# Optimization experiments

Hardware: AMD Instinct MI355X
Metric: run time of the kernel (lower is better)

## Reference

```python
import jax, jax.numpy as jnp
import numpy as np

# Production-scale dims: total AST nodes, total CFG nodes, number of mapping pairs
N_AST, N_CFG, M = 500_000, 100_000, 400_000
D_AST, D_CFG = 256, 256


def setup_inputs() -> dict:
    key = jax.random.key(0)
    ks = jax.random.split(key, 6)
    prev = jax.random.normal(ks[0], (N_AST, D_AST), jnp.float32)
    cfg = jax.random.normal(ks[1], (N_CFG, D_CFG), jnp.float32)
    # unique key indices (a random subset of AST node ids) -> deterministic scatter
    key_indices = jax.random.permutation(ks[2], N_AST)[:M].astype(jnp.int32)
    value_indices = jax.random.randint(ks[3], (M,), 0, N_CFG, jnp.int32)
    s_u = 1.0 / np.sqrt(D_CFG)
    W_update = jax.random.uniform(ks[4], (D_CFG, D_AST), jnp.float32, -s_u, s_u)
    b_update = jnp.zeros((D_AST,), jnp.float32)
    s_g = 1.0 / np.sqrt(2 * D_AST)
    W_gate = jax.random.uniform(ks[5], (2 * D_AST, D_AST), jnp.float32, -s_g, s_g)
    b_gate = jnp.zeros((D_AST,), jnp.float32)
    return dict(
        previous_ast_nodes_encodings=prev,
        new_cfg_nodes_encodings=cfg,
        key_indices=key_indices,
        value_indices=value_indices,
        W_update=W_update,
        b_update=b_update,
        W_gate=W_gate,
        b_gate=b_gate,
    )


def reference(previous_ast_nodes_encodings, new_cfg_nodes_encodings,
              key_indices, value_indices, W_update, b_update, W_gate, b_gate):
    # gather: rows of AST-node state and CFG-node updates participating in the mapping
    state = previous_ast_nodes_encodings[key_indices]      # [M, D_AST]
    upd = new_cfg_nodes_encodings[value_indices]           # [M, D_CFG]
    # StateUpdater (gated update; dropout is identity in eval mode)
    proj = jax.nn.relu(upd @ W_update + b_update)          # project update to state dim
    gate = jax.nn.sigmoid(jnp.concatenate([state, proj], axis=-1) @ W_gate + b_gate)
    new_state = gate * state + (1.0 - gate) * proj         # [M, D_AST]
    # scatter updated rows back into the full AST-node encodings tensor
    return previous_ast_nodes_encodings.at[key_indices].set(new_state)
```

## Files before the change

kernel.cpp:

```cpp
#include <hip/hip_runtime.h>
#include <hip/hip_bf16.h>

typedef __attribute__((ext_vector_type(8))) short short8;
typedef __attribute__((ext_vector_type(4))) float f32x4;
typedef __attribute__((ext_vector_type(4))) unsigned short u16x4;

#define D 256

static __device__ __forceinline__ unsigned short f2bf(float f) {
    union { __hip_bfloat16 h; unsigned short u; } v;
    v.h = __float2bfloat16(f);
    return v.u;
}
static __device__ __forceinline__ float bf2f(unsigned short h) {
    union { unsigned u; float f; } v; v.u = ((unsigned)h) << 16;
    return v.f;
}

__global__ void pack_w_kernel(const float* __restrict__ W, unsigned short* __restrict__ dst,
                              int log2nkk, int total) {
    int p = blockIdx.x * blockDim.x + threadIdx.x;
    if (p >= total) return;
    int j     = p & 7;
    int lane  = (p >> 3) & 63;
    int kk    = (p >> 9) & ((1 << log2nkk) - 1);
    int ntile = p >> (9 + log2nkk);
    int k = kk * 32 + ((lane >> 4) * 8) + j;
    int n = ntile * 16 + (lane & 15);
    dst[p] = f2bf(W[k * D + n]);
}

__global__ void clear_flags_kernel(unsigned* __restrict__ f, int n) {
    int i = blockIdx.x * blockDim.x + threadIdx.x;
    if (i < n) f[i] = 0u;
}

__global__ void scatter_flags_kernel(const int* __restrict__ kidx,
                                     unsigned char* __restrict__ flags, int m) {
    int i = blockIdx.x * blockDim.x + threadIdx.x;
    if (i < m) flags[kidx[i]] = 1;
}

__global__ void copy_rows_kernel(const f32x4* __restrict__ src, f32x4* __restrict__ dst,
                                 const unsigned char* __restrict__ flags, int nrows) {
    int w    = (blockIdx.x * blockDim.x + threadIdx.x) >> 6;
    int lane = threadIdx.x & 63;
    int nw   = (gridDim.x * blockDim.x) >> 6;
    for (int row = w; row < nrows; row += nw) {
        if (flags[row]) continue;
        size_t idx = (size_t)row * 64 + lane;
        f32x4 v = __builtin_nontemporal_load(src + idx);
        __builtin_nontemporal_store(v, dst + idx);
    }
}

__global__ __launch_bounds__(256, 5) void projall_kernel(
    const float* __restrict__ cfg, const unsigned short* __restrict__ WuP,
    const float* __restrict__ bu, unsigned short* __restrict__ projall, int ncfg)
{
    __shared__ unsigned short Aub[64 * D];
    char* aubB = (char*)Aub;
    const int t = threadIdx.x, lane = t & 63, wid = t >> 6;
    const int lr = lane & 15, lk = lane >> 4;
    const int base = blockIdx.x * 64;

    #pragma unroll
    for (int i = 0; i < 16; ++i) {
        int row = wid * 16 + i;
        int r = base + row;
        f32x4 u = (f32x4){0.f, 0.f, 0.f, 0.f};
        if (r < ncfg) u = *(const f32x4*)(cfg + (size_t)r * D + lane * 4);
        int boff = (lane * 8) ^ ((row & 7) << 4);
        u16x4 hu;
        hu.x = f2bf(u.x); hu.y = f2bf(u.y); hu.z = f2bf(u.z); hu.w = f2bf(u.w);
        *(u16x4*)(aubB + row * 512 + boff) = hu;
    }
    __syncthreads();

    f32x4 acc[4][4];
    #pragma unroll
    for (int fm = 0; fm < 4; ++fm)
        #pragma unroll
        for (int fn = 0; fn < 4; ++fn)
            acc[fm][fn] = (f32x4){0.f, 0.f, 0.f, 0.f};

    #pragma unroll
    for (int kk = 0; kk < 8; ++kk) {
        short8 a[4], b[4];
        #pragma unroll
        for (int fm = 0; fm < 4; ++fm) {
            int row = fm * 16 + lr;
            int boff = (kk * 64 + lk * 16) ^ ((row & 7) << 4);
            a[fm] = *(const short8*)(aubB + row * 512 + boff);
        }
        #pragma unroll
        for (int fn = 0; fn < 4; ++fn) {
            int ntile = wid * 4 + fn;
            b[fn] = *(const short8*)(WuP + ((size_t)(ntile * 8 + kk) * 64 + lane) * 8);
        }
        #pragma unroll
        for (int fm = 0; fm < 4; ++fm)
            #pragma unroll
            for (int fn = 0; fn < 4; ++fn)
                acc[fm][fn] = __builtin_amdgcn_mfma_f32_16x16x32_bf16(a[fm], b[fn], acc[fm][fn], 0, 0, 0);
    }

    float bu4[4];
    #pragma unroll
    for (int fn = 0; fn < 4; ++fn) bu4[fn] = bu[wid * 64 + fn * 16 + lr];

    #pragma unroll
    for (int fm = 0; fm < 4; ++fm) {
        #pragma unroll
        for (int i = 0; i < 4; ++i) {
            int r = base + fm * 16 + lk * 4 + i;
            if (r >= ncfg) continue;
            #pragma unroll
            for (int fn = 0; fn < 4; ++fn) {
                float p = acc[fm][fn][i] + bu4[fn];
                p = p > 0.f ? p : 0.f;
                projall[(size_t)r * D + wid * 64 + fn * 16 + lr] = f2bf(p);
            }
        }
    }
}

__global__ __launch_bounds__(512, 4) void fused2_kernel(
    const float* __restrict__ prev, const unsigned short* __restrict__ projall,
    const int* __restrict__ kidx, const int* __restrict__ vidx,
    const unsigned short* __restrict__ WgP, const float* __restrict__ bg,
    float* __restrict__ out)
{
    __shared__ unsigned short Ast[64 * D];
    __shared__ unsigned short Apj[64 * D];
    char* astB = (char*)Ast;
    char* apjB = (char*)Apj;

    const int t    = threadIdx.x;
    const int lane = t & 63;
    const int wid  = t >> 6;
    const int lr   = lane & 15;
    const int lk   = lane >> 4;
    const int base = blockIdx.x * 64;

    #pragma unroll
    for (int i = 0; i < 8; ++i) {
        int row = wid * 8 + i;
        int kr = kidx[base + row];
        f32x4 s = __builtin_nontemporal_load((const f32x4*)(prev + (size_t)kr * D) + lane);
        int boff = (lane * 8) ^ ((row & 7) << 4);
        u16x4 hs;
        hs.x = f2bf(s.x); hs.y = f2bf(s.y); hs.z = f2bf(s.z); hs.w = f2bf(s.w);
        *(u16x4*)(astB + row * 512 + boff) = hs;
    }
    #pragma unroll
    for (int i = 0; i < 4; ++i) {
        int row = wid * 8 + i * 2 + (lane >> 5);
        int vr = vidx[base + row];
        short8 pv = *(const short8*)(projall + (size_t)vr * D + (lane & 31) * 8);
        int boff = ((lane & 31) * 16) ^ ((row & 7) << 4);
        *(short8*)(apjB + row * 512 + boff) = pv;
    }
    __syncthreads();

    f32x4 acc2[4][2];
    #pragma unroll
    for (int fm = 0; fm < 4; ++fm)
        #pragma unroll
        for (int fn = 0; fn < 2; ++fn)
            acc2[fm][fn] = (f32x4){0.f, 0.f, 0.f, 0.f};

    #pragma unroll
    for (int kk = 0; kk < 16; ++kk) {
        const char* Asrc = (kk < 8) ? astB : apjB;
        int kkl = kk & 7;
        short8 a[4], b[2];
        #pragma unroll
        for (int fm = 0; fm < 4; ++fm) {
            int row = fm * 16 + lr;
            int boff = (kkl * 64 + lk * 16) ^ ((row & 7) << 4);
            a[fm] = *(const short8*)(Asrc + row * 512 + boff);
        }
        #pragma unroll
        for (int fn = 0; fn < 2; ++fn) {
            int ntile = wid * 2 + fn;
            b[fn] = *(const short8*)(WgP + ((size_t)(ntile * 16 + kk) * 64 + lane) * 8);
        }
        #pragma unroll
        for (int fm = 0; fm < 4; ++fm)
            #pragma unroll
            for (int fn = 0; fn < 2; ++fn)
                acc2[fm][fn] = __builtin_amdgcn_mfma_f32_16x16x32_bf16(a[fm], b[fn], acc2[fm][fn], 0, 0, 0);
    }

    float bg2[2];
    #pragma unroll
    for (int fn = 0; fn < 2; ++fn) bg2[fn] = bg[wid * 32 + fn * 16 + lr];

    #pragma unroll
    for (int fm = 0; fm < 4; ++fm) {
        #pragma unroll
        for (int i = 0; i < 4; ++i) {
            int row = fm * 16 + lk * 4 + i;
            int kr = kidx[base + row];
            float* orow = out + (size_t)kr * D;
            #pragma unroll
            for (int fn = 0; fn < 2; ++fn) {
                int col = wid * 32 + fn * 16 + lr;
                float x = acc2[fm][fn][i] + bg2[fn];
                float g = 1.f / (1.f + __expf(-x));
                int boff = (col * 2) ^ ((row & 7) << 4);
                float st = bf2f(*(const unsigned short*)(astB + row * 512 + boff));
                float pj = bf2f(*(const unsigned short*)(apjB + row * 512 + boff));
                __builtin_nontemporal_store(g * st + (1.f - g) * pj, orow + col);
            }
        }
    }
}

__global__ __launch_bounds__(256, 5) void fused_kernel(
    const float* __restrict__ prev, const float* __restrict__ cfg,
    const int* __restrict__ kidx, const int* __restrict__ vidx,
    const unsigned short* __restrict__ WuP, const unsigned short* __restrict__ WgP,
    const float* __restrict__ bu, const float* __restrict__ bg,
    float* __restrict__ out)
{
    __shared__ unsigned short Ast[32 * D];
    __shared__ unsigned short Aub[32 * D];
    char* astB = (char*)Ast;
    char* aubB = (char*)Aub;
    const int t = threadIdx.x, lane = t & 63, wid = t >> 6;
    const int lr = lane & 15, lk = lane >> 4;
    const int base = blockIdx.x * 32;

    #pragma unroll
    for (int i = 0; i < 8; ++i) {
        int row = wid * 8 + i;
        int kr = kidx[base + row];
        int vr = vidx[base + row];
        f32x4 s = *(const f32x4*)(prev + (size_t)kr * D + lane * 4);
        f32x4 u = *(const f32x4*)(cfg  + (size_t)vr * D + lane * 4);
        int boff = (lane * 8) ^ ((row & 7) << 4);
        u16x4 hs, hu;
        hs.x = f2bf(s.x); hs.y = f2bf(s.y); hs.z = f2bf(s.z); hs.w = f2bf(s.w);
        hu.x = f2bf(u.x); hu.y = f2bf(u.y); hu.z = f2bf(u.z); hu.w = f2bf(u.w);
        *(u16x4*)(astB + row * 512 + boff) = hs;
        *(u16x4*)(aubB + row * 512 + boff) = hu;
    }
    __syncthreads();

    f32x4 acc[2][4];
    #pragma unroll
    for (int fm = 0; fm < 2; ++fm)
        #pragma unroll
        for (int fn = 0; fn < 4; ++fn) acc[fm][fn] = (f32x4){0.f,0.f,0.f,0.f};

    #pragma unroll
    for (int kk = 0; kk < 8; ++kk) {
        short8 a[2], b[4];
        #pragma unroll
        for (int fm = 0; fm < 2; ++fm) {
            int row = fm * 16 + lr;
            int boff = (kk * 64 + lk * 16) ^ ((row & 7) << 4);
            a[fm] = *(const short8*)(aubB + row * 512 + boff);
        }
        #pragma unroll
        for (int fn = 0; fn < 4; ++fn)
            b[fn] = *(const short8*)(WuP + ((size_t)((wid*4+fn) * 8 + kk) * 64 + lane) * 8);
        #pragma unroll
        for (int fm = 0; fm < 2; ++fm)
            #pragma unroll
            for (int fn = 0; fn < 4; ++fn)
                acc[fm][fn] = __builtin_amdgcn_mfma_f32_16x16x32_bf16(a[fm], b[fn], acc[fm][fn], 0, 0, 0);
    }

    float bu4[4];
    #pragma unroll
    for (int fn = 0; fn < 4; ++fn) bu4[fn] = bu[wid * 64 + fn * 16 + lr];
    __syncthreads();

    #pragma unroll
    for (int fm = 0; fm < 2; ++fm)
        #pragma unroll
        for (int fn = 0; fn < 4; ++fn)
            #pragma unroll
            for (int i = 0; i < 4; ++i) {
                float p = acc[fm][fn][i] + bu4[fn];
                p = p > 0.f ? p : 0.f;
                int row = fm * 16 + lk * 4 + i;
                int col = wid * 64 + fn * 16 + lr;
                *(unsigned short*)(aubB + row * 512 + ((col*2) ^ ((row&7)<<4))) = f2bf(p);
            }
    __syncthreads();

    f32x4 acc2[2][4];
    #pragma unroll
    for (int fm = 0; fm < 2; ++fm)
        #pragma unroll
        for (int fn = 0; fn < 4; ++fn) acc2[fm][fn] = (f32x4){0.f,0.f,0.f,0.f};

    #pragma unroll
    for (int kk = 0; kk < 16; ++kk) {
        const char* Asrc = (kk < 8) ? astB : aubB;
        int kkl = kk & 7;
        short8 a[2], b[4];
        #pragma unroll
        for (int fm = 0; fm < 2; ++fm) {
            int row = fm * 16 + lr;
            int boff = (kkl * 64 + lk * 16) ^ ((row & 7) << 4);
            a[fm] = *(const short8*)(Asrc + row * 512 + boff);
        }
        #pragma unroll
        for (int fn = 0; fn < 4; ++fn)
            b[fn] = *(const short8*)(WgP + ((size_t)((wid*4+fn) * 16 + kk) * 64 + lane) * 8);
        #pragma unroll
        for (int fm = 0; fm < 2; ++fm)
            #pragma unroll
            for (int fn = 0; fn < 4; ++fn)
                acc2[fm][fn] = __builtin_amdgcn_mfma_f32_16x16x32_bf16(a[fm], b[fn], acc2[fm][fn], 0, 0, 0);
    }

    float bg4[4];
    #pragma unroll
    for (int fn = 0; fn < 4; ++fn) bg4[fn] = bg[wid * 64 + fn * 16 + lr];

    #pragma unroll
    for (int fm = 0; fm < 2; ++fm)
        #pragma unroll
        for (int i = 0; i < 4; ++i) {
            int row = fm * 16 + lk * 4 + i;
            int kr = kidx[base + row];
            float* orow = out + (size_t)kr * D;
            #pragma unroll
            for (int fn = 0; fn < 4; ++fn) {
                int col = wid * 64 + fn * 16 + lr;
                float x = acc2[fm][fn][i] + bg4[fn];
                float g = 1.f / (1.f + __expf(-x));
                int boff = (col * 2) ^ ((row & 7) << 4);
                float st = bf2f(*(const unsigned short*)(astB + row * 512 + boff));
                float pj = bf2f(*(const unsigned short*)(aubB + row * 512 + boff));
                orow[col] = g * st + (1.f - g) * pj;
            }
        }
}

extern "C" void kernel_launch(void* const* d_in, const int* in_sizes, int n_in,
                              void* d_out, int out_size, void* d_ws, size_t ws_size,
                              hipStream_t stream) {
    const float* prev = (const float*)d_in[0];
    const float* cfg  = (const float*)d_in[1];
    const int* kidx   = (const int*)d_in[2];
    const int* vidx   = (const int*)d_in[3];
    const float* Wu   = (const float*)d_in[4];
    const float* bu   = (const float*)d_in[5];
    const float* Wg   = (const float*)d_in[6];
    const float* bg   = (const float*)d_in[7];
    float* out = (float*)d_out;

    const int N_AST = in_sizes[0] / D;
    const int N_CFG = in_sizes[1] / D;
    const int M     = in_sizes[2];

    unsigned short* WuP = (unsigned short*)d_ws;
    unsigned short* WgP = WuP + 256 * 256;
    unsigned char* flags = (unsigned char*)(WgP + 512 * 256);
    unsigned short* projall = (unsigned short*)((char*)d_ws + (1 << 20));

    const int totalWu = 256 * 256;
    const int totalWg = 512 * 256;
    const int nflag4  = (N_AST + 3) / 4;
    const size_t needed = (size_t)(1 << 20) + (size_t)N_CFG * D * 2;

    pack_w_kernel<<<(totalWu + 255) / 256, 256, 0, stream>>>(Wu, WuP, 3, totalWu);
    pack_w_kernel<<<(totalWg + 255) / 256, 256, 0, stream>>>(Wg, WgP, 4, totalWg);
    clear_flags_kernel<<<(nflag4 + 255) / 256, 256, 0, stream>>>((unsigned*)flags, nflag4);
    scatter_flags_kernel<<<(M + 255) / 256, 256, 0, stream>>>(kidx, flags, M);

    if (ws_size >= needed) {
        projall_kernel<<<(N_CFG + 63) / 64, 256, 0, stream>>>(cfg, WuP, bu, projall, N_CFG);
        fused2_kernel<<<M / 64, 512, 0, stream>>>(prev, projall, kidx, vidx, WgP, bg, out);
    } else {
        fused_kernel<<<M / 32, 256, 0, stream>>>(prev, cfg, kidx, vidx, WuP, WgP, bu, bg, out);
    }
    copy_rows_kernel<<<2048, 256, 0, stream>>>((const f32x4*)prev, (f32x4*)out, flags, N_AST);
}
```

Baseline: 392.4 us.

## Make gate kernel persistent with register-prefetched gathers for next tile

Replaces the one-block-per-tile gate kernel with a persistent grid of 512 blocks that loop over 64-row tiles. While the current tile's MFMA and epilogue run, each block prefetches the next tile's gathered state rows and projected rows into registers, so gather latency overlaps compute. It also removes the fallback path that skipped the precomputed projection when the workspace was too small, so the workspace size is now assumed to be enough. The register prefetch buffers add pressure and could lower occupancy, and the fixed grid may leave some CUs unevenly loaded.

```diff
diff --git a/kernel.cpp b/kernel.cpp
--- a/kernel.cpp
+++ b/kernel.cpp
@@ -125,223 +125,134 @@
     }
 }
 
-__global__ __launch_bounds__(512, 4) void fused2_kernel(
+__global__ __launch_bounds__(512, 4) void fused3_kernel(
     const float* __restrict__ prev, const unsigned short* __restrict__ projall,
     const int* __restrict__ kidx, const int* __restrict__ vidx,
     const unsigned short* __restrict__ WgP, const float* __restrict__ bg,
-    float* __restrict__ out)
+    float* __restrict__ out, int ntiles)
 {
     __shared__ unsigned short Ast[64 * D];
     __shared__ unsigned short Apj[64 * D];
     char* astB = (char*)Ast;
     char* apjB = (char*)Apj;
 
-    const int t    = threadIdx.x;
-    const int lane = t & 63;
-    const int wid  = t >> 6;
+    const int tid  = threadIdx.x;
+    const int lane = tid & 63;
+    const int wid  = tid >> 6;
     const int lr   = lane & 15;
     const int lk   = lane >> 4;
-    const int base = blockIdx.x * 64;
-
-    #pragma unroll
-    for (int i = 0; i < 8; ++i) {
-        int row = wid * 8 + i;
-        int kr = kidx[base + row];
-        f32x4 s = __builtin_nontemporal_load((const f32x4*)(prev + (size_t)kr * D) + lane);
-        int boff = (lane * 8) ^ ((row & 7) << 4);
-        u16x4 hs;
-        hs.x = f2bf(s.x); hs.y = f2bf(s.y); hs.z = f2bf(s.z); hs.w = f2bf(s.w);
-        *(u16x4*)(astB + row * 512 + boff) = hs;
-    }
-    #pragma unroll
-    for (int i = 0; i < 4; ++i) {
-        int row = wid * 8 + i * 2 + (lane >> 5);
-        int vr = vidx[base + row];
-        short8 pv = *(const short8*)(projall + (size_t)vr * D + (lane & 31) * 8);
-        int boff = ((lane & 31) * 16) ^ ((row & 7) << 4);
-        *(short8*)(apjB + row * 512 + boff) = pv;
-    }
-    __syncthreads();
-
-    f32x4 acc2[4][2];
-    #pragma unroll
-    for (int fm = 0; fm < 4; ++fm)
-        #pragma unroll
-        for (int fn = 0; fn < 2; ++fn)
-            acc2[fm][fn] = (f32x4){0.f, 0.f, 0.f, 0.f};
-
-    #pragma unroll
-    for (int kk = 0; kk < 16; ++kk) {
-        const char* Asrc = (kk < 8) ? astB : apjB;
-        int kkl = kk & 7;
-        short8 a[4], b[2];
+    const int t0   = blockIdx.x;
+    const int step = gridDim.x;
+
+    float bg2[2];
+    #pragma unroll
+    for (int fn = 0; fn < 2; ++fn) bg2[fn] = bg[wid * 32 + fn * 16 + lr];
+
+    f32x4 sreg[8];
+    short8 preg[4];
+
+    {
+        int base = t0 * 64;
+        #pragma unroll
+        for (int i = 0; i < 8; ++i) {
+            int kr = kidx[base + wid * 8 + i];
+            sreg[i] = __builtin_nontemporal_load((const f32x4*)(prev + (size_t)kr * D) + lane);
+        }
+        #pragma unroll
+        for (int i = 0; i < 4; ++i) {
+            int row = wid * 8 + i * 2 + (lane >> 5);
+            int vr = vidx[base + row];
+            preg[i] = *(const short8*)(projall + (size_t)vr * D + (lane & 31) * 8);
+        }
+    }
+
+    for (int t = t0; t < ntiles; t += step) {
+        const int base = t * 64;
+
+        #pragma unroll
+        for (int i = 0; i < 8; ++i) {
+            int row = wid * 8 + i;
+            int boff = (lane * 8) ^ ((row & 7) << 4);
+            u16x4 hs;
+            hs.x = f2bf(sreg[i].x); hs.y = f2bf(sreg[i].y);
+            hs.z = f2bf(sreg[i].z); hs.w = f2bf(sreg[i].w);
+            *(u16x4*)(astB + row * 512 + boff) = hs;
+        }
+        #pragma unroll
+        for (int i = 0; i < 4; ++i) {
+            int row = wid * 8 + i * 2 + (lane >> 5);
+            int boff = ((lane & 31) * 16) ^ ((row & 7) << 4);
+            *(short8*)(apjB + row * 512 + boff) = preg[i];
+        }
+        __syncthreads();
+
+        int tn = t + step;
+        if (tn < ntiles) {
+            int nbase = tn * 64;
+            #pragma unroll
+            for (int i = 0; i < 8; ++i) {
+                int kr = kidx[nbase + wid * 8 + i];
+                sreg[i] = __builtin_nontemporal_load((const f32x4*)(prev + (size_t)kr * D) + lane);
+            }
+            #pragma unroll
+            for (int i = 0; i < 4; ++i) {
+                int row = wid * 8 + i * 2 + (lane >> 5);
+                int vr = vidx[nbase + row];
+                preg[i] = *(const short8*)(projall + (size_t)vr * D + (lane & 31) * 8);
+            }
+        }
+
+        f32x4 acc2[4][2];
+        #pragma unroll
+        for (int fm = 0; fm < 4; ++fm)
+            #pragma unroll
+            for (int fn = 0; fn < 2; ++fn)
+                acc2[fm][fn] = (f32x4){0.f, 0.f, 0.f, 0.f};
+
+        #pragma unroll
+        for (int kk = 0; kk < 16; ++kk) {
+            const char* Asrc = (kk < 8) ? astB : apjB;
+            int kkl = kk & 7;
+            short8 a[4], b[2];
+            #pragma unroll
+            for (int fm = 0; fm < 4; ++fm) {
+                int row = fm * 16 + lr;
+                int boff = (kkl * 64 + lk * 16) ^ ((row & 7) << 4);
+                a[fm] = *(const short8*)(Asrc + row * 512 + boff);
+            }
+            #pragma unroll
+            for (int fn = 0; fn < 2; ++fn) {
+                int ntile = wid * 2 + fn;
+                b[fn] = *(const short8*)(WgP + ((size_t)(ntile * 16 + kk) * 64 + lane) * 8);
+            }
+            #pragma unroll
+            for (int fm = 0; fm < 4; ++fm)
+                #pragma unroll
+                for (int fn = 0; fn < 2; ++fn)
+                    acc2[fm][fn] = __builtin_amdgcn_mfma_f32_16x16x32_bf16(a[fm], b[fn], acc2[fm][fn], 0, 0, 0);
+        }
+
         #pragma unroll
         for (int fm = 0; fm < 4; ++fm) {
-            int row = fm * 16 + lr;
-            int boff = (kkl * 64 + lk * 16) ^ ((row & 7) << 4);
-            a[fm] = *(const short8*)(Asrc + row * 512 + boff);
-        }
-        #pragma unroll
-        for (int fn = 0; fn < 2; ++fn) {
-            int ntile = wid * 2 + fn;
-            b[fn] = *(const short8*)(WgP + ((size_t)(ntile * 16 + kk) * 64 + lane) * 8);
-        }
-        #pragma unroll
-        for (int fm = 0; fm < 4; ++fm)
-            #pragma unroll
-            for (int fn = 0; fn < 2; ++fn)
-                acc2[fm][fn] = __builtin_amdgcn_mfma_f32_16x16x32_bf16(a[fm], b[fn], acc2[fm][fn], 0, 0, 0);
-    }
-
-    float bg2[2];
-    #pragma unroll
-    for (int fn = 0; fn < 2; ++fn) bg2[fn] = bg[wid * 32 + fn * 16 + lr];
-
-    #pragma unroll
-    for (int fm = 0; fm < 4; ++fm) {
-        #pragma unroll
-        for (int i = 0; i < 4; ++i) {
-            int row = fm * 16 + lk * 4 + i;
-            int kr = kidx[base + row];
-            float* orow = out + (size_t)kr * D;
-            #pragma unroll
-            for (int fn = 0; fn < 2; ++fn) {
-                int col = wid * 32 + fn * 16 + lr;
-                float x = acc2[fm][fn][i] + bg2[fn];
-                float g = 1.f / (1.f + __expf(-x));
-                int boff = (col * 2) ^ ((row & 7) << 4);
-                float st = bf2f(*(const unsigned short*)(astB + row * 512 + boff));
-                float pj = bf2f(*(const unsigned short*)(apjB + row * 512 + boff));
-                __builtin_nontemporal_store(g * st + (1.f - g) * pj, orow + col);
-            }
-        }
-    }
-}
-
-__global__ __launch_bounds__(256, 5) void fused_kernel(
-    const float* __restrict__ prev, const float* __restrict__ cfg,
-    const int* __restrict__ kidx, const int* __restrict__ vidx,
-    const unsigned short* __restrict__ WuP, const unsigned short* __restrict__ WgP,
-    const float* __restrict__ bu, const float* __restrict__ bg,
-    float* __restrict__ out)
-{
-    __shared__ unsigned short Ast[32 * D];
-    __shared__ unsigned short Aub[32 * D];
-    char* astB = (char*)Ast;
-    char* aubB = (char*)Aub;
-    const int t = threadIdx.x, lane = t & 63, wid = t >> 6;
-    const int lr = lane & 15, lk = lane >> 4;
-    const int base = blockIdx.x * 32;
-
-    #pragma unroll
-    for (int i = 0; i < 8; ++i) {
-        int row = wid * 8 + i;
-        int kr = kidx[base + row];
-        int vr = vidx[base + row];
-        f32x4 s = *(const f32x4*)(prev + (size_t)kr * D + lane * 4);
-        f32x4 u = *(const f32x4*)(cfg  + (size_t)vr * D + lane * 4);
-        int boff = (lane * 8) ^ ((row & 7) << 4);
-        u16x4 hs, hu;
-        hs.x = f2bf(s.x); hs.y = f2bf(s.y); hs.z = f2bf(s.z); hs.w = f2bf(s.w);
-        hu.x = f2bf(u.x); hu.y = f2bf(u.y); hu.z = f2bf(u.z); hu.w = f2bf(u.w);
-        *(u16x4*)(astB + row * 512 + boff) = hs;
-        *(u16x4*)(aubB + row * 512 + boff) = hu;
-    }
-    __syncthreads();
-
-    f32x4 acc[2][4];
-    #pragma unroll
-    for (int fm = 0; fm < 2; ++fm)
-        #pragma unroll
-        for (int fn = 0; fn < 4; ++fn) acc[fm][fn] = (f32x4){0.f,0.f,0.f,0.f};
-
-    #pragma unroll
-    for (int kk = 0; kk < 8; ++kk) {
-        short8 a[2], b[4];
-        #pragma unroll
-        for (int fm = 0; fm < 2; ++fm) {
-            int row = fm * 16 + lr;
-            int boff = (kk * 64 + lk * 16) ^ ((row & 7) << 4);
-            a[fm] = *(const short8*)(aubB + row * 512 + boff);
-        }
-        #pragma unroll
-        for (int fn = 0; fn < 4; ++fn)
-            b[fn] = *(const short8*)(WuP + ((size_t)((wid*4+fn) * 8 + kk) * 64 + lane) * 8);
-        #pragma unroll
-        for (int fm = 0; fm < 2; ++fm)
-            #pragma unroll
-            for (int fn = 0; fn < 4; ++fn)
-                acc[fm][fn] = __builtin_amdgcn_mfma_f32_16x16x32_bf16(a[fm], b[fn], acc[fm][fn], 0, 0, 0);
-    }
-
-    float bu4[4];
-    #pragma unroll
-    for (int fn = 0; fn < 4; ++fn) bu4[fn] = bu[wid * 64 + fn * 16 + lr];
-    __syncthreads();
-
-    #pragma unroll
-    for (int fm = 0; fm < 2; ++fm)
-        #pragma unroll
-        for (int fn = 0; fn < 4; ++fn)
             #pragma unroll
             for (int i = 0; i < 4; ++i) {
-                float p = acc[fm][fn][i] + bu4[fn];
-                p = p > 0.f ? p : 0.f;
                 int row = fm * 16 + lk * 4 + i;
-                int col = wid * 64 + fn * 16 + lr;
-                *(unsigned short*)(aubB + row * 512 + ((col*2) ^ ((row&7)<<4))) = f2bf(p);
-            }
-    __syncthreads();
-
-    f32x4 acc2[2][4];
-    #pragma unroll
-    for (int fm = 0; fm < 2; ++fm)
-        #pragma unroll
-        for (int fn = 0; fn < 4; ++fn) acc2[fm][fn] = (f32x4){0.f,0.f,0.f,0.f};
-
-    #pragma unroll
-    for (int kk = 0; kk < 16; ++kk) {
-        const char* Asrc = (kk < 8) ? astB : aubB;
-        int kkl = kk & 7;
-        short8 a[2], b[4];
-        #pragma unroll
-        for (int fm = 0; fm < 2; ++fm) {
-            int row = fm * 16 + lr;
-            int boff = (kkl * 64 + lk * 16) ^ ((row & 7) << 4);
-            a[fm] = *(const short8*)(Asrc + row * 512 + boff);
-        }
-        #pragma unroll
-        for (int fn = 0; fn < 4; ++fn)
-            b[fn] = *(const short8*)(WgP + ((size_t)((wid*4+fn) * 16 + kk) * 64 + lane) * 8);
-        #pragma unroll
-        for (int fm = 0; fm < 2; ++fm)
-            #pragma unroll
-            for (int fn = 0; fn < 4; ++fn)
-                acc2[fm][fn] = __builtin_amdgcn_mfma_f32_16x16x32_bf16(a[fm], b[fn], acc2[fm][fn], 0, 0, 0);
-    }
-
-    float bg4[4];
-    #pragma unroll
-    for (int fn = 0; fn < 4; ++fn) bg4[fn] = bg[wid * 64 + fn * 16 + lr];
-
-    #pragma unroll
-    for (int fm = 0; fm < 2; ++fm)
-        #pragma unroll
-        for (int i = 0; i < 4; ++i) {
-            int row = fm * 16 + lk * 4 + i;
-            int kr = kidx[base + row];
-            float* orow = out + (size_t)kr * D;
-            #pragma unroll
-            for (int fn = 0; fn < 4; ++fn) {
-                int col = wid * 64 + fn * 16 + lr;
-                float x = acc2[fm][fn][i] + bg4[fn];
-                float g = 1.f / (1.f + __expf(-x));
-                int boff = (col * 2) ^ ((row & 7) << 4);
-                float st = bf2f(*(const unsigned short*)(astB + row * 512 + boff));
-                float pj = bf2f(*(const unsigned short*)(aubB + row * 512 + boff));
-                orow[col] = g * st + (1.f - g) * pj;
-            }
-        }
+                int kr = kidx[base + row];
+                float* orow = out + (size_t)kr * D;
+                #pragma unroll
+                for (int fn = 0; fn < 2; ++fn) {
+                    int col = wid * 32 + fn * 16 + lr;
+                    float x = acc2[fm][fn][i] + bg2[fn];
+                    float g = 1.f / (1.f + __expf(-x));
+                    int boff = (col * 2) ^ ((row & 7) << 4);
+                    float st = bf2f(*(const unsigned short*)(astB + row * 512 + boff));
+                    float pj = bf2f(*(const unsigned short*)(apjB + row * 512 + boff));
+                    __builtin_nontemporal_store(g * st + (1.f - g) * pj, orow + col);
+                }
+            }
+        }
+        __syncthreads();
+    }
 }
 
 extern "C" void kernel_launch(void* const* d_in, const int* in_sizes, int n_in,
@@ -369,18 +280,14 @@
     const int totalWu = 256 * 256;
     const int totalWg = 512 * 256;
     const int nflag4  = (N_AST + 3) / 4;
-    const size_t needed = (size_t)(1 << 20) + (size_t)N_CFG * D * 2;
+    const int ntiles  = M / 64;
 
     pack_w_kernel<<<(totalWu + 255) / 256, 256, 0, stream>>>(Wu, WuP, 3, totalWu);
     pack_w_kernel<<<(totalWg + 255) / 256, 256, 0, stream>>>(Wg, WgP, 4, totalWg);
     clear_flags_kernel<<<(nflag4 + 255) / 256, 256, 0, stream>>>((unsigned*)flags, nflag4);
     scatter_flags_kernel<<<(M + 255) / 256, 256, 0, stream>>>(kidx, flags, M);
 
-    if (ws_size >= needed) {
-        projall_kernel<<<(N_CFG + 63) / 64, 256, 0, stream>>>(cfg, WuP, bu, projall, N_CFG);
-        fused2_kernel<<<M / 64, 512, 0, stream>>>(prev, projall, kidx, vidx, WgP, bg, out);
-    } else {
-        fused_kernel<<<M / 32, 256, 0, stream>>>(prev, cfg, kidx, vidx, WuP, WgP, bu, bg, out);
-    }
+    projall_kernel<<<(N_CFG + 63) / 64, 256, 0, stream>>>(cfg, WuP, bu, projall, N_CFG);
+    fused3_kernel<<<512, 512, 0, stream>>>(prev, projall, kidx, vidx, WgP, bg, out, ntiles);
     copy_rows_kernel<<<2048, 256, 0, stream>>>((const f32x4*)prev, (f32x4*)out, flags, N_AST);
 }
```

After: 1.015 ms. 159% more time.
